# Optimization experiments

Measured on AMD Instinct MI355X. Metric: run time of the kernel, lower is better.

The kernel has to match this reference:

```python
import jax, jax.numpy as jnp
import numpy as np

B, S, I, H, O = 128, 1024, 256, 512, 10


def setup_inputs() -> dict:
    key = jax.random.key(0)
    ks = jax.random.split(key, 7)
    s_ih = 1.0 / np.sqrt(H)
    return {
        "x": jax.random.normal(ks[0], (B, S, I), dtype=jnp.float32),
        "W_ih": jax.random.uniform(ks[1], (4 * H, I), minval=-s_ih, maxval=s_ih, dtype=jnp.float32),
        "W_hh": jax.random.uniform(ks[2], (4 * H, H), minval=-s_ih, maxval=s_ih, dtype=jnp.float32),
        "b_ih": jax.random.uniform(ks[3], (4 * H,), minval=-s_ih, maxval=s_ih, dtype=jnp.float32),
        "b_hh": jax.random.uniform(ks[4], (4 * H,), minval=-s_ih, maxval=s_ih, dtype=jnp.float32),
        "fc_w": jax.random.uniform(ks[5], (O, H), minval=-s_ih, maxval=s_ih, dtype=jnp.float32),
        "fc_b": jax.random.uniform(ks[6], (O,), minval=-s_ih, maxval=s_ih, dtype=jnp.float32),
    }


def reference(x, W_ih, W_hh, b_ih, b_hh, fc_w, fc_b):
    batch = x.shape[0]
    hid = W_hh.shape[1]
    # Precompute input projections for all timesteps: [S, B, 4H]
    x_proj = jnp.einsum("bsi,gi->sbg", x, W_ih) + b_ih + b_hh

    def step(carry, xp_t):
        h, c = carry
        gates = xp_t + h @ W_hh.T  # [B, 4H]
        yi, yf, yg, yo = jnp.split(gates, 4, axis=-1)
        i_gate = jax.nn.sigmoid(yi)
        f_gate = jax.nn.sigmoid(yf)
        g_gate = jax.nn.relu(yg)
        o_gate = jax.nn.sigmoid(yo)
        c = f_gate * c + i_gate * g_gate
        h = o_gate * c  # note: no tanh on c (custom variant)
        return (h, c), None

    h0 = jnp.zeros((batch, hid), dtype=x.dtype)
    c0 = jnp.zeros((batch, hid), dtype=x.dtype)
    (h, _), _ = jax.lax.scan(step, (h0, c0), x_proj)
    # dropout is identity in eval / p=0
    return h @ fc_w.T + fc_b
```

## Files before the change

kernel.cpp:

```cpp
#include <hip/hip_runtime.h>
#include <stdint.h>


#define GROUPS 8
#define BC     16
#define S_LEN  1024
#define I_DIM  256
#define H_DIM  512
#define NBLK   512
#define FSTRIDE 16
#define SUBSTRIDE 64
#define PAYG   (BC * H_DIM)
#define PAYSLOT (GROUPS * PAYG)

typedef float f32x4 __attribute__((ext_vector_type(4)));
typedef short s16x8 __attribute__((ext_vector_type(8)));
typedef unsigned u32x4 __attribute__((ext_vector_type(4)));

__device__ __forceinline__ unsigned short f2bf(float f) {
  unsigned u = __float_as_uint(f);
  u += 0x7fffu + ((u >> 16) & 1u);
  return (unsigned short)(u >> 16);
}
__device__ __forceinline__ float bf2f(unsigned short h) {
  return __uint_as_float(((unsigned)h) << 16);
}
__device__ __forceinline__ float sigf(float x) { return 1.0f / (1.0f + __expf(-x)); }

__device__ __forceinline__ unsigned cvt_pk_bf16(float lo, float hi) {
  unsigned r;
  asm("v_cvt_pk_bf16_f32 %0, %1, %2" : "=v"(r) : "v"(lo), "v"(hi));
  return r;
}

__device__ __forceinline__ int poll_local(uint64_t a) {
  int v;
  asm volatile("global_atomic_add %0, %1, %2, off sc0\n\ts_waitcnt vmcnt(0)"
               : "=v"(v) : "v"(a), "v"(0) : "memory");
  return v;
}
__device__ __forceinline__ int ld_sc1(uint64_t a) {
  int v;
  asm volatile("global_load_dword %0, %1, off sc1\n\ts_waitcnt vmcnt(0)"
               : "=v"(v) : "v"(a) : "memory");
  return v;
}
__device__ __forceinline__ void st_sc1(uint64_t a, int v) {
  asm volatile("global_store_dword %0, %1, off sc1" :: "v"(a), "v"(v) : "memory");
}
__device__ __forceinline__ void drain_vm() {
  asm volatile("s_waitcnt vmcnt(0)" ::: "memory");
}

__global__ __launch_bounds__(256, 2)
void lstm_persistent(const float* __restrict__ x,
                     const float* __restrict__ Wih,
                     const float* __restrict__ Whh,
                     const float* __restrict__ bih,
                     const float* __restrict__ bhh,
                     const float* __restrict__ fcw,
                     const float* __restrict__ fcb,
                     float* __restrict__ out,
                     int* __restrict__ arrive,
                     int* __restrict__ table,
                     int* __restrict__ flags,
                     unsigned short* __restrict__ hpay,
                     int wmask)
{
  __shared__ __align__(16) unsigned short x_s[2][8][512];
  __shared__ __align__(16) unsigned short h_stage[8192];
  __shared__ __align__(16) float gates[4][BC][18];
  __shared__ int tbl[NBLK];
  __shared__ unsigned long long seen[GROUPS][4];
  __shared__ int s_grp, s_slot, s_abort;

  const int tid  = threadIdx.x;
  const int wave = tid >> 6;
  const int lane = tid & 63;
  const int q    = lane >> 4;
  const int l15  = lane & 15;
  const int bid  = blockIdx.x;

  const int xcd = __builtin_amdgcn_s_getreg((31u << 11) | 20) & 7;
  const int cuk = __builtin_amdgcn_s_getreg((7u << 11) | (8u << 6) | 4) & 0xff;
  if (tid == 0) {
    st_sc1((uint64_t)&table[bid], xcd | (cuk << 3));
    drain_vm();
    atomicAdd(arrive, 1);
    int spins = 0;
    while (atomicAdd(arrive, 0) < NBLK && spins < (1 << 22)) {
      __builtin_amdgcn_s_sleep(8);
      ++spins;
    }
  }
  if (tid < 32) *(unsigned long long*)&seen[tid >> 2][tid & 3] = 0ull;
  __syncthreads();
  tbl[tid]       = ld_sc1((uint64_t)&table[tid]);
  tbl[tid + 256] = ld_sc1((uint64_t)&table[tid + 256]);
  __syncthreads();
  if (tid == 0) {
    int cnt[8]    = {0, 0, 0, 0, 0, 0, 0, 0};
    int wcount[8] = {0, 0, 0, 0, 0, 0, 0, 0};
    int my_rank = 0, my_w = -1;
    for (int j = 0; j < NBLK; ++j) {
      const int e  = tbl[j];
      const int xx = e & 7;
      const int ky = (e >> 3) & 0xff;
      const unsigned long long bit = 1ull << (ky & 63);
      const bool first = !(seen[xx][ky >> 6] & bit);
      if (first) seen[xx][ky >> 6] |= bit;
      int w = -1;
      if (first && wcount[xx] < 32) w = wcount[xx]++;
      if (j == bid) { my_rank = cnt[xx]; my_w = w; }
      cnt[xx]++;
    }
    int slot = my_w;
    if (wcount[xcd] != 32)
      slot = (my_rank < 32) ? my_rank : -1;
    s_grp = (slot >= 0) ? xcd : -1;
    s_slot = slot;
    s_abort = 0;
  }
  __syncthreads();
  const int g    = s_grp;
  const int slot = s_slot;
  if (g < 0) return;

  const int gcol = wave * H_DIM + slot * 16 + l15;
  s16x8 bhh_f[16];
#pragma unroll
  for (int kb = 0; kb < 16; ++kb) {
    const float* src = Whh + (size_t)gcol * H_DIM + kb * 32 + q * 8;
    s16x8 v;
#pragma unroll
    for (int i = 0; i < 8; ++i) v[i] = (short)f2bf(src[i]);
    bhh_f[kb] = v;
  }
  s16x8 bih_f[8];
#pragma unroll
  for (int kb = 0; kb < 8; ++kb) {
    const float* src = Wih + (size_t)gcol * I_DIM + kb * 32 + q * 8;
    s16x8 v;
#pragma unroll
    for (int i = 0; i < 8; ++i) v[i] = (short)f2bf(src[i]);
    bih_f[kb] = v;
  }
  const float bias_v = bih[gcol] + bhh[gcol];

  const int m0  = tid & 15;
  const int kc0 = tid >> 4;
  const int xkb   = kc0 >> 1;
  const int laneA = m0 + 32 * (kc0 & 1);
  const int laneB = laneA + 16;
  const float* const xrow = x + (size_t)(g * BC + m0) * S_LEN * I_DIM + kc0 * 16;

  {
    float xt[16];
    *(float4*)&xt[0]  = ((const float4*)xrow)[0];
    *(float4*)&xt[4]  = ((const float4*)xrow)[1];
    *(float4*)&xt[8]  = ((const float4*)xrow)[2];
    *(float4*)&xt[12] = ((const float4*)xrow)[3];
    u32x4 v0, v1;
#pragma unroll
    for (int i = 0; i < 4; ++i) {
      v0[i] = cvt_pk_bf16(xt[2 * i],     xt[2 * i + 1]);
      v1[i] = cvt_pk_bf16(xt[8 + 2 * i], xt[8 + 2 * i + 1]);
    }
    *(u32x4*)&x_s[0][xkb][laneA * 8] = v0;
    *(u32x4*)&x_s[0][xkb][laneB * 8] = v1;
  }
  float xN[16];
  {
    const float* src = xrow + (size_t)1 * I_DIM;
    *(float4*)&xN[0]  = ((const float4*)src)[0];
    *(float4*)&xN[4]  = ((const float4*)src)[1];
    *(float4*)&xN[8]  = ((const float4*)src)[2];
    *(float4*)&xN[12] = ((const float4*)src)[3];
  }
  __syncthreads();

  int* const gcnt = flags + (size_t)g * 32 * FSTRIDE;

  const int erow  = wave * 4 + q;
  const int kcol  = slot * 16 + l15;
  const int sidx  = (kcol >> 5) * 512 + (erow + 16 * ((kcol >> 3) & 3)) * 8 + (kcol & 7);

  int p = 0;
  float c_reg = 0.0f;

  for (int t = 0; t < S_LEN; ++t) {
    if (t + 1 < S_LEN) {
      u32x4 v0, v1;
#pragma unroll
      for (int i = 0; i < 4; ++i) {
        v0[i] = cvt_pk_bf16(xN[2 * i],     xN[2 * i + 1]);
        v1[i] = cvt_pk_bf16(xN[8 + 2 * i], xN[8 + 2 * i + 1]);
      }
      *(u32x4*)&x_s[p ^ 1][xkb][laneA * 8] = v0;
      *(u32x4*)&x_s[p ^ 1][xkb][laneB * 8] = v1;
    }

    if (t + 2 < S_LEN) {
      const float* src = xrow + (size_t)(t + 2) * I_DIM;
      *(float4*)&xN[0]  = ((const float4*)src)[0];
      *(float4*)&xN[4]  = ((const float4*)src)[1];
      *(float4*)&xN[8]  = ((const float4*)src)[2];
      *(float4*)&xN[12] = ((const float4*)src)[3];
    }

    f32x4 acc = {bias_v, bias_v, bias_v, bias_v};
#pragma unroll
    for (int kb = 0; kb < 8; ++kb) {
      s16x8 a = *(const s16x8*)&x_s[p][kb][lane * 8];
      acc = __builtin_amdgcn_mfma_f32_16x16x32_bf16(a, bih_f[kb], acc, 0, 0, 0);
    }

    if (t > 0) {
      if (tid < 4 && !s_abort) {
        const uint64_t a = (uint64_t)(gcnt + (size_t)tid * SUBSTRIDE);
        const int need = 8 * t;
        int rounds = 0;
        for (;;) {
          int v = poll_local(a);
          if (__all(v >= need)) break;
          if (++rounds > (1 << 16)) { if (tid == 0) s_abort = 1; break; }
          __builtin_amdgcn_s_sleep(2);
        }
      }
      __syncthreads();
      {
        const unsigned short* pb =
            hpay + (size_t)((t & wmask) * GROUPS + g) * PAYG + (size_t)tid * 8;
        s16x8 c0 = *(const s16x8*)(pb);
        s16x8 c1 = *(const s16x8*)(pb + 2048);
        s16x8 c2 = *(const s16x8*)(pb + 4096);
        s16x8 c3 = *(const s16x8*)(pb + 6144);
        *(s16x8*)&h_stage[tid * 8]        = c0;
        *(s16x8*)&h_stage[tid * 8 + 2048] = c1;
        *(s16x8*)&h_stage[tid * 8 + 4096] = c2;
        *(s16x8*)&h_stage[tid * 8 + 6144] = c3;
      }
      __syncthreads();
      f32x4 h0 = {0.f, 0.f, 0.f, 0.f}, h1 = {0.f, 0.f, 0.f, 0.f};
#pragma unroll
      for (int kb = 0; kb < 16; kb += 2) {
        const s16x8 a0 = *(const s16x8*)&h_stage[(kb    ) * 512 + lane * 8];
        const s16x8 a1 = *(const s16x8*)&h_stage[(kb + 1) * 512 + lane * 8];
        h0 = __builtin_amdgcn_mfma_f32_16x16x32_bf16(a0, bhh_f[kb],     h0, 0, 0, 0);
        h1 = __builtin_amdgcn_mfma_f32_16x16x32_bf16(a1, bhh_f[kb + 1], h1, 0, 0, 0);
      }
      acc += h0 + h1;
    }

#pragma unroll
    for (int r = 0; r < 4; ++r) gates[wave][q * 4 + r][l15] = acc[r];
    __syncthreads();

    {
      float yi = gates[0][erow][l15];
      float yf = gates[1][erow][l15];
      float yg = gates[2][erow][l15];
      float yo = gates[3][erow][l15];
      float ig = sigf(yi), fg = sigf(yf), gg = fmaxf(yg, 0.0f), og = sigf(yo);
      c_reg = fg * c_reg + ig * gg;
      float h = og * c_reg;
      hpay[(size_t)(((t + 1) & wmask) * GROUPS + g) * PAYG + sidx] =
          (unsigned short)cvt_pk_bf16(h, h);
    }

    drain_vm();
    __syncthreads();
    if (tid == 0) atomicAdd(gcnt + (size_t)(slot & 3) * SUBSTRIDE, 1);

    p ^= 1;
  }

  if (slot == 0) {
    if (tid < 4 && !s_abort) {
      const uint64_t a = (uint64_t)(gcnt + (size_t)tid * SUBSTRIDE);
      const int need = 8 * S_LEN;
      int rounds = 0;
      for (;;) {
        int v = poll_local(a);
        if (__all(v >= need)) break;
        if (++rounds > (1 << 16)) break;
        __builtin_amdgcn_s_sleep(2);
      }
    }
    __syncthreads();
    unsigned short* hfc = &x_s[0][0][0];
    {
      const unsigned short* pb = hpay + (size_t)g * PAYG + (size_t)tid * 32;
      s16x8 cc[4];
      cc[0] = ((const s16x8*)pb)[0];
      cc[1] = ((const s16x8*)pb)[1];
      cc[2] = ((const s16x8*)pb)[2];
      cc[3] = ((const s16x8*)pb)[3];
      const int kb = tid >> 4;
      const int L0 = (tid & 15) * 4;
#pragma unroll
      for (int i = 0; i < 4; ++i) {
        const int L = L0 + i;
        const int m = L & 15, qq = L >> 4;
        *(s16x8*)&hfc[m * 512 + kb * 32 + qq * 8] = cc[i];
      }
    }
    __syncthreads();

    if (tid < BC * 10) {
      const int row = tid / 10, o = tid - row * 10;
      const float* wr = fcw + (size_t)o * H_DIM;
      float sum = fcb[o];
      for (int k = 0; k < H_DIM; k += 8) {
#pragma unroll
        for (int j = 0; j < 8; ++j)
          sum += bf2f(hfc[row * 512 + k + j]) * wr[k + j];
      }
      out[(g * BC + row) * 10 + o] = sum;
    }
  }
}

extern "C" void kernel_launch(void* const* d_in, const int* in_sizes, int n_in,
                              void* d_out, int out_size, void* d_ws, size_t ws_size,
                              hipStream_t stream) {
  (void)in_sizes; (void)n_in; (void)out_size;
  const float* x   = (const float*)d_in[0];
  const float* Wih = (const float*)d_in[1];
  const float* Whh = (const float*)d_in[2];
  const float* bih = (const float*)d_in[3];
  const float* bhh = (const float*)d_in[4];
  const float* fcw = (const float*)d_in[5];
  const float* fcb = (const float*)d_in[6];

  int* arrive = (int*)d_ws;
  int* table  = (int*)((char*)d_ws + 4096);
  int* flags  = (int*)((char*)d_ws + 8192);
  unsigned short* hpay = (unsigned short*)((char*)d_ws + 32768);

  size_t avail = ws_size > 32768 ? ws_size - 32768 : 0;
  int W = 2;
  while (W < 16 && (size_t)(W * 2) * (PAYSLOT * 2) <= avail) W <<= 1;

  hipMemsetAsync(d_ws, 0, 32768, stream);

  hipLaunchKernelGGL(lstm_persistent, dim3(NBLK), dim3(256), 0, stream,
                     x, Wih, Whh, bih, bhh, fcw, fcb, (float*)d_out,
                     arrive, table, flags, hpay, W - 1);
}
```

Measured before the change: 2.317 ms.

## Replace atomic counter barrier with per-block flag stores and spin polling

Each block in a group now stores its step index to its own flag slot instead of atomically incrementing one of four shared counters. Waiters poll all 32 flags with one lane each, using mostly non-temporal loads and an atomic read every fourth round, and no longer sleep between polls. This removes atomic contention and the sleep latency on the critical per-timestep barrier. The cost is more polling traffic, and correctness depends on the plain flag stores and nt loads staying visible and ordered across CUs.

Measured after the change: 2.296 ms. No clear change (-0.9%).

```diff
diff --git a/kernel.cpp b/kernel.cpp
--- a/kernel.cpp
+++ b/kernel.cpp
@@ -9,7 +9,6 @@
 #define H_DIM  512
 #define NBLK   512
 #define FSTRIDE 16
-#define SUBSTRIDE 64
 #define PAYG   (BC * H_DIM)
 #define PAYSLOT (GROUPS * PAYG)
 
@@ -39,6 +38,12 @@
                : "=v"(v) : "v"(a), "v"(0) : "memory");
   return v;
 }
+__device__ __forceinline__ int poll_nt(uint64_t a) {
+  int v;
+  asm volatile("global_load_dword %0, %1, off nt\n\ts_waitcnt vmcnt(0)"
+               : "=v"(v) : "v"(a) : "memory");
+  return v;
+}
 __device__ __forceinline__ int ld_sc1(uint64_t a) {
   int v;
   asm volatile("global_load_dword %0, %1, off sc1\n\ts_waitcnt vmcnt(0)"
@@ -47,6 +52,9 @@
 }
 __device__ __forceinline__ void st_sc1(uint64_t a, int v) {
   asm volatile("global_store_dword %0, %1, off sc1" :: "v"(a), "v"(v) : "memory");
+}
+__device__ __forceinline__ void st_flag(uint64_t a, int v) {
+  asm volatile("global_store_dword %0, %1, off" :: "v"(a), "v"(v) : "memory");
 }
 __device__ __forceinline__ void drain_vm() {
   asm volatile("s_waitcnt vmcnt(0)" ::: "memory");
@@ -179,7 +187,9 @@
   }
   __syncthreads();
 
-  int* const gcnt = flags + (size_t)g * 32 * FSTRIDE;
+  int* const     fgrp  = flags + (size_t)g * 32 * FSTRIDE;
+  const uint64_t fpoll = (uint64_t)(fgrp + (size_t)(tid & 31) * FSTRIDE);
+  const uint64_t fmine = (uint64_t)(fgrp + (size_t)slot * FSTRIDE);
 
   const int erow  = wave * 4 + q;
   const int kcol  = slot * 16 + l15;
@@ -216,15 +226,12 @@
     }
 
     if (t > 0) {
-      if (tid < 4 && !s_abort) {
-        const uint64_t a = (uint64_t)(gcnt + (size_t)tid * SUBSTRIDE);
-        const int need = 8 * t;
+      if (tid < 32 && !s_abort) {
         int rounds = 0;
         for (;;) {
-          int v = poll_local(a);
-          if (__all(v >= need)) break;
+          int v = ((rounds & 3) == 3) ? poll_local(fpoll) : poll_nt(fpoll);
+          if (__all(v >= t)) break;
           if (++rounds > (1 << 16)) { if (tid == 0) s_abort = 1; break; }
-          __builtin_amdgcn_s_sleep(2);
         }
       }
       __syncthreads();
@@ -270,21 +277,18 @@
 
     drain_vm();
     __syncthreads();
-    if (tid == 0) atomicAdd(gcnt + (size_t)(slot & 3) * SUBSTRIDE, 1);
+    if (tid == 0) st_flag(fmine, t + 1);
 
     p ^= 1;
   }
 
   if (slot == 0) {
-    if (tid < 4 && !s_abort) {
-      const uint64_t a = (uint64_t)(gcnt + (size_t)tid * SUBSTRIDE);
-      const int need = 8 * S_LEN;
+    if (tid < 32 && !s_abort) {
       int rounds = 0;
       for (;;) {
-        int v = poll_local(a);
-        if (__all(v >= need)) break;
+        int v = ((rounds & 3) == 3) ? poll_local(fpoll) : poll_nt(fpoll);
+        if (__all(v >= S_LEN)) break;
         if (++rounds > (1 << 16)) break;
-        __builtin_amdgcn_s_sleep(2);
       }
     }
     __syncthreads();
```
